# Kernel optimization log

Measured on AMD Instinct MI355X. Metric: run time of the kernel, lower is better.

Reference implementation:

```python
import jax, jax.numpy as jnp
import numpy as np

DIM = 512
HEADS = 8
HEAD_DIM = DIM // HEADS
SCALING = float(np.sqrt(HEAD_DIM))
B, S = 8, 2048


def setup_inputs() -> dict:
    key = jax.random.key(0)
    ks = jax.random.split(key, 6)
    x = jax.random.normal(ks[0], (B, S, DIM), dtype=jnp.float32)
    mask = jax.random.randint(ks[1], (B, S), 0, 2).astype(bool)
    mask = mask.at[:, 0].set(False)  # guarantee at least one unmasked key per row
    lim_qkv = 1.0 / np.sqrt(DIM)
    Wqkv = jax.random.uniform(ks[2], (3 * DIM, DIM), minval=-lim_qkv, maxval=lim_qkv, dtype=jnp.float32)
    bqkv = jax.random.uniform(ks[3], (3 * DIM,), minval=-lim_qkv, maxval=lim_qkv, dtype=jnp.float32)
    Wout = jax.random.uniform(ks[4], (DIM, DIM), minval=-lim_qkv, maxval=lim_qkv, dtype=jnp.float32)
    bout = jax.random.uniform(ks[5], (DIM,), minval=-lim_qkv, maxval=lim_qkv, dtype=jnp.float32)
    ln_g = jnp.ones((DIM,), dtype=jnp.float32)
    ln_b = jnp.zeros((DIM,), dtype=jnp.float32)
    return {"x": x, "mask": mask, "Wqkv": Wqkv, "bqkv": bqkv, "Wout": Wout, "bout": bout, "ln_g": ln_g, "ln_b": ln_b}


def reference(x, mask, Wqkv, bqkv, Wout, bout, ln_g, ln_b):
    b, s, _ = x.shape
    qkv = x @ Wqkv.T + bqkv                                   # [b, s, 3*dim]
    qkv = qkv.reshape(b, s, HEADS, HEAD_DIM, 3)               # torch reshape semantics (interleaved)
    q = qkv[..., 0]                                           # [b, s, h, d]
    k = qkv[..., 1]
    v = jax.nn.elu(qkv[..., 2])
    attn = jnp.einsum('bqhd,bkhd->bhqk', q, k) / SCALING      # [b, h, s, s]
    bias = jnp.where(mask[:, None, None, :], -jnp.inf, 0.0).astype(attn.dtype)
    attn = jax.nn.softmax(attn + bias, axis=-1)
    out = jnp.einsum('bhqk,bkhd->bqhd', attn, v).reshape(b, s, DIM)
    out = out @ Wout.T + bout
    mu = jnp.mean(out, axis=-1, keepdims=True)
    var = jnp.var(out, axis=-1, keepdims=True)
    out = (out - mu) / jnp.sqrt(var + 1e-5) * ln_g + ln_b
    return jax.nn.elu(out)
```

## Files before the change

kernel.cpp:

```cpp
#include <hip/hip_runtime.h>

#define DIM 512
#define HEADS 8
#define HD 64
#define NB 8
#define NS 2048
#define SCALE_INV 0.125f
#define NEG_BIG -1e30f
#define QSZ 8388608

typedef __attribute__((ext_vector_type(8))) short bf16x8;
typedef __attribute__((ext_vector_type(4))) float f32x4;

__device__ __forceinline__ float elu_f(float x) {
    return x > 0.0f ? x : (__expf(x) - 1.0f);
}
__device__ __forceinline__ short f2bf(float x) {
    union { float f; unsigned u; } v; v.f = x;
    unsigned r = v.u + 0x7FFFu + ((v.u >> 16) & 1u);
    return (short)(r >> 16);
}
__device__ __forceinline__ unsigned pack_bf_t(float a, float b) {
    union { float f; unsigned u; } va, vb; va.f = a; vb.f = b;
    return (va.u >> 16) | (vb.u & 0xFFFF0000u);
}

#define X4 2097152
#define W14 196608
#define W24 65536
__global__ __launch_bounds__(256) void prep(
    const float* __restrict__ x, const float* __restrict__ Wqkv,
    const float* __restrict__ bqkv, const float* __restrict__ Wout,
    short* __restrict__ xb, short* __restrict__ Wp,
    float* __restrict__ bp, short* __restrict__ Wob)
{
    int i = blockIdx.x * 256 + threadIdx.x;
    if (i < X4) {
        float4 v = *(const float4*)(x + (size_t)i * 4);
        ushort4 o; o.x = (unsigned short)f2bf(v.x); o.y = (unsigned short)f2bf(v.y);
        o.z = (unsigned short)f2bf(v.z); o.w = (unsigned short)f2bf(v.w);
        *(ushort4*)(xb + (size_t)i * 4) = o;
    } else if (i < X4 + W14) {
        int j = i - X4;
        int np = j >> 7, k = (j & 127) * 4;
        int w = np >> 9, h = (np >> 6) & 7, d = np & 63;
        int n = h * 192 + d * 3 + w;
        float4 v = *(const float4*)(Wqkv + (size_t)n * 512 + k);
        ushort4 o; o.x = (unsigned short)f2bf(v.x); o.y = (unsigned short)f2bf(v.y);
        o.z = (unsigned short)f2bf(v.z); o.w = (unsigned short)f2bf(v.w);
        *(ushort4*)(Wp + (size_t)np * 512 + k) = o;
    } else if (i < X4 + W14 + W24) {
        int j = i - X4 - W14;
        float4 v = *(const float4*)(Wout + (size_t)j * 4);
        ushort4 o; o.x = (unsigned short)f2bf(v.x); o.y = (unsigned short)f2bf(v.y);
        o.z = (unsigned short)f2bf(v.z); o.w = (unsigned short)f2bf(v.w);
        *(ushort4*)(Wob + (size_t)j * 4) = o;
    } else {
        int j = i - X4 - W14 - W24;
        int w = j >> 9, h = (j >> 6) & 7, d = j & 63;
        bp[j] = bqkv[h * 192 + d * 3 + w];
    }
}

__global__ __launch_bounds__(256) void qkv_mfma(
    const short* __restrict__ A, const short* __restrict__ Bw,
    const float* __restrict__ bp, short* __restrict__ QKV)
{
    __shared__ short smem[2 * 128 * 64];
    short* As = smem;
    short* Bs = smem + 128 * 64;
    const int t = threadIdx.x, lane = t & 63, wv = t >> 6;
    const int c = lane & 15, quad = lane >> 4;
    const int wr = wv >> 1, wc = wv & 1;
    const int m0 = blockIdx.x * 128, n0 = blockIdx.y * 128;
    f32x4 acc[4][4];
    #pragma unroll
    for (int mi = 0; mi < 4; ++mi)
        #pragma unroll
        for (int nj = 0; nj < 4; ++nj)
            #pragma unroll
            for (int i = 0; i < 4; ++i) acc[mi][nj][i] = 0.0f;

    for (int k0 = 0; k0 < 512; k0 += 64) {
        if (k0) __syncthreads();
        #pragma unroll
        for (int p = 0; p < 4; ++p) {
            int idx = p * 256 + t, r = idx >> 3, cb = idx & 7;
            *(uint4*)&As[r * 64 + ((cb ^ (r & 7)) * 8)] =
                *(const uint4*)(A + (size_t)(m0 + r) * 512 + k0 + cb * 8);
            *(uint4*)&Bs[r * 64 + ((cb ^ (r & 7)) * 8)] =
                *(const uint4*)(Bw + (size_t)(n0 + r) * 512 + k0 + cb * 8);
        }
        __syncthreads();
        bf16x8 af[4][2], bfr[4][2];
        #pragma unroll
        for (int mi = 0; mi < 4; ++mi) {
            int ar = wr * 64 + mi * 16 + c;
            af[mi][0] = *(const bf16x8*)&As[ar * 64 + ((quad       ^ (ar & 7)) * 8)];
            af[mi][1] = *(const bf16x8*)&As[ar * 64 + (((4 + quad) ^ (ar & 7)) * 8)];
        }
        #pragma unroll
        for (int nj = 0; nj < 4; ++nj) {
            int br = wc * 64 + nj * 16 + c;
            bfr[nj][0] = *(const bf16x8*)&Bs[br * 64 + ((quad       ^ (br & 7)) * 8)];
            bfr[nj][1] = *(const bf16x8*)&Bs[br * 64 + (((4 + quad) ^ (br & 7)) * 8)];
        }
        #pragma unroll
        for (int mi = 0; mi < 4; ++mi)
            #pragma unroll
            for (int nj = 0; nj < 4; ++nj) {
                acc[mi][nj] = __builtin_amdgcn_mfma_f32_16x16x32_bf16(af[mi][0], bfr[nj][0], acc[mi][nj], 0, 0, 0);
                acc[mi][nj] = __builtin_amdgcn_mfma_f32_16x16x32_bf16(af[mi][1], bfr[nj][1], acc[mi][nj], 0, 0, 0);
            }
    }

    const int w  = n0 >> 9;
    const int b  = m0 >> 11;
    const int hh = ((n0 + wc * 64) >> 6) & 7;
    float bv[4];
    #pragma unroll
    for (int nj = 0; nj < 4; ++nj) bv[nj] = bp[n0 + wc * 64 + nj * 16 + c];

    if (w < 2) {
        short* out = QKV + (size_t)w * QSZ + (size_t)(b * 8 + hh) * NS * 64;
        #pragma unroll
        for (int mi = 0; mi < 4; ++mi)
            #pragma unroll
            for (int i = 0; i < 4; ++i) {
                int s = (m0 & (NS - 1)) + wr * 64 + mi * 16 + quad * 4 + i;
                #pragma unroll
                for (int nj = 0; nj < 4; ++nj)
                    out[(size_t)s * 64 + nj * 16 + c] = f2bf(acc[mi][nj][i] + bv[nj]);
            }
    } else {
        __syncthreads();
        short* T = smem;
        #pragma unroll
        for (int mi = 0; mi < 4; ++mi)
            #pragma unroll
            for (int i = 0; i < 4; ++i) {
                int ml = wr * 64 + mi * 16 + quad * 4 + i;
                int mb = ml >> 3, mr = ml & 7;
                #pragma unroll
                for (int nj = 0; nj < 4; ++nj) {
                    int nl = wc * 64 + nj * 16 + c;
                    T[nl * 128 + ((mb ^ (nl & 15)) * 8) + mr] =
                        f2bf(elu_f(acc[mi][nj][i] + bv[nj]));
                }
            }
        __syncthreads();
        short* Vt = QKV + (size_t)2 * QSZ;
        #pragma unroll
        for (int p = 0; p < 8; ++p) {
            int idx = p * 256 + t, row = idx >> 4, ch = idx & 15;
            uint4 v = *(const uint4*)&T[row * 128 + ((ch ^ (row & 15)) * 8)];
            int d = row & 63;
            int h2 = ((n0 + row) >> 6) & 7;
            int sg = (m0 & (NS - 1)) + ch * 8;
            int kt = sg >> 6, ks = sg & 63;
            *(uint4*)(Vt + (((size_t)(b * 8 + h2) * 32 + kt) * 64 + d) * 64 + ks) = v;
        }
    }
}

__global__ __launch_bounds__(256, 4) void attn_mfma(
    const short* __restrict__ Qg, const short* __restrict__ Kg,
    const short* __restrict__ Vg, const int* __restrict__ mask,
    short* __restrict__ O)
{
    __shared__ short QP[64 * 64];
    __shared__ short Ks[64 * 64];
    __shared__ short Vs[64 * 64];
    __shared__ float msk[64];

    const int t = threadIdx.x;
    const int lane = t & 63;
    const int wv = t >> 6;
    const int c = lane & 15;
    const int quad = lane >> 4;
    const int bid = blockIdx.x;
    const int qt = bid & 31;
    const int h  = (bid >> 5) & 7;
    const int b  = bid >> 8;
    const int g  = b * 8 + h;
    const size_t base = (size_t)g * NS * HD;
    const int q0 = qt * 64;

    #pragma unroll
    for (int p = 0; p < 2; ++p) {
        int idx = p * 256 + t, r = idx >> 3, cb = idx & 7;
        *(uint4*)&QP[r * 64 + ((cb ^ (r & 7)) * 8)] =
            *(const uint4*)(Qg + base + (size_t)(q0 + r) * HD + cb * 8);
    }
    __syncthreads();

    const int mq = wv * 16 + c;
    const bf16x8 bq0 = *(const bf16x8*)&QP[mq * 64 + ((quad       ^ (mq & 7)) * 8)];
    const bf16x8 bq1 = *(const bf16x8*)&QP[mq * 64 + (((4 + quad) ^ (mq & 7)) * 8)];

    f32x4 o[4];
    #pragma unroll
    for (int dc = 0; dc < 4; ++dc)
        #pragma unroll
        for (int i = 0; i < 4; ++i) o[dc][i] = 0.0f;
    float lp = 0.0f;

    const int prow = wv * 16 + c;
    const int prot = 8 * (c & 7);

    for (int kt = 0; kt < 32; ++kt) {
        const int k0 = kt * 64;
        __syncthreads();
        #pragma unroll
        for (int p = 0; p < 2; ++p) {
            int idx = p * 256 + t, r = idx >> 3, cb = idx & 7;
            *(uint4*)&Ks[r * 64 + ((cb ^ (r & 7)) * 8)] =
                *(const uint4*)(Kg + base + (size_t)(k0 + r) * HD + cb * 8);
            *(uint4*)&Vs[r * 64 + (((cb * 8 + 8 * (r & 7)) & 63))] =
                *(const uint4*)(Vg + (((size_t)g * 32 + kt) * 64 + r) * 64 + cb * 8);
        }
        if (t < 64) msk[t] = mask[b * NS + k0 + t] ? NEG_BIG : 0.0f;
        __syncthreads();

        f32x4 st[4];
        #pragma unroll
        for (int ks = 0; ks < 4; ++ks) {
            int kr = ks * 16 + c;
            bf16x8 ak0 = *(const bf16x8*)&Ks[kr * 64 + ((quad       ^ (kr & 7)) * 8)];
            bf16x8 ak1 = *(const bf16x8*)&Ks[kr * 64 + (((4 + quad) ^ (kr & 7)) * 8)];
            f32x4 a = {0.0f, 0.0f, 0.0f, 0.0f};
            a = __builtin_amdgcn_mfma_f32_16x16x32_bf16(ak0, bq0, a, 0, 0, 0);
            a = __builtin_amdgcn_mfma_f32_16x16x32_bf16(ak1, bq1, a, 0, 0, 0);
            st[ks] = a;
        }

        #pragma unroll
        for (int ks = 0; ks < 4; ++ks) {
            float4 mb = *(const float4*)&msk[ks * 16 + quad * 4];
            float p0 = __expf(st[ks][0] * SCALE_INV + mb.x);
            float p1 = __expf(st[ks][1] * SCALE_INV + mb.y);
            float p2 = __expf(st[ks][2] * SCALE_INV + mb.z);
            float p3 = __expf(st[ks][3] * SCALE_INV + mb.w);
            lp += (p0 + p1) + (p2 + p3);
            uint2 pk;
            pk.x = pack_bf_t(p0, p1);
            pk.y = pack_bf_t(p2, p3);
            *(uint2*)&QP[prow * 64 + ((ks * 16 + quad * 4 + prot) & 63)] = pk;
        }

        bf16x8 bp0 = *(const bf16x8*)&QP[prow * 64 + ((quad * 8 + prot) & 63)];
        bf16x8 bp1 = *(const bf16x8*)&QP[prow * 64 + ((32 + quad * 8 + prot) & 63)];
        #pragma unroll
        for (int dc = 0; dc < 4; ++dc) {
            int d = dc * 16 + c;
            int vrot = 8 * (d & 7);
            bf16x8 av0 = *(const bf16x8*)&Vs[d * 64 + ((quad * 8 + vrot) & 63)];
            bf16x8 av1 = *(const bf16x8*)&Vs[d * 64 + ((32 + quad * 8 + vrot) & 63)];
            o[dc] = __builtin_amdgcn_mfma_f32_16x16x32_bf16(av0, bp0, o[dc], 0, 0, 0);
            o[dc] = __builtin_amdgcn_mfma_f32_16x16x32_bf16(av1, bp1, o[dc], 0, 0, 0);
        }
    }

    lp += __shfl_xor(lp, 16);
    lp += __shfl_xor(lp, 32);
    float inv = 1.0f / lp;

    int q = q0 + wv * 16 + c;
    short* orow = O + ((size_t)(b * NS + q)) * DIM + h * HD + quad * 4;
    #pragma unroll
    for (int dc = 0; dc < 4; ++dc) {
        uint2 pk;
        pk.x = (unsigned)(unsigned short)f2bf(o[dc][0] * inv)
             | ((unsigned)(unsigned short)f2bf(o[dc][1] * inv) << 16);
        pk.y = (unsigned)(unsigned short)f2bf(o[dc][2] * inv)
             | ((unsigned)(unsigned short)f2bf(o[dc][3] * inv) << 16);
        *(uint2*)(orow + dc * 16) = pk;
    }
}

__global__ __launch_bounds__(256) void out_mfma(
    const short* __restrict__ A, const short* __restrict__ Bw,
    const float* __restrict__ bias, float* __restrict__ Z)
{
    __shared__ short smem[2 * 128 * 64];
    short* As = smem;
    short* Bs = smem + 128 * 64;
    const int t = threadIdx.x, lane = t & 63, wv = t >> 6;
    const int c = lane & 15, quad = lane >> 4;
    const int wr = wv >> 1, wc = wv & 1;
    const int m0 = blockIdx.x * 128, n0 = blockIdx.y * 128;
    f32x4 acc[4][4];
    #pragma unroll
    for (int mi = 0; mi < 4; ++mi)
        #pragma unroll
        for (int nj = 0; nj < 4; ++nj)
            #pragma unroll
            for (int i = 0; i < 4; ++i) acc[mi][nj][i] = 0.0f;

    for (int k0 = 0; k0 < 512; k0 += 64) {
        if (k0) __syncthreads();
        #pragma unroll
        for (int p = 0; p < 4; ++p) {
            int idx = p * 256 + t, r = idx >> 3, cb = idx & 7;
            *(uint4*)&As[r * 64 + ((cb ^ (r & 7)) * 8)] =
                *(const uint4*)(A + (size_t)(m0 + r) * 512 + k0 + cb * 8);
            *(uint4*)&Bs[r * 64 + ((cb ^ (r & 7)) * 8)] =
                *(const uint4*)(Bw + (size_t)(n0 + r) * 512 + k0 + cb * 8);
        }
        __syncthreads();
        bf16x8 af[4][2], bfr[4][2];
        #pragma unroll
        for (int mi = 0; mi < 4; ++mi) {
            int ar = wr * 64 + mi * 16 + c;
            af[mi][0] = *(const bf16x8*)&As[ar * 64 + ((quad       ^ (ar & 7)) * 8)];
            af[mi][1] = *(const bf16x8*)&As[ar * 64 + (((4 + quad) ^ (ar & 7)) * 8)];
        }
        #pragma unroll
        for (int nj = 0; nj < 4; ++nj) {
            int br = wc * 64 + nj * 16 + c;
            bfr[nj][0] = *(const bf16x8*)&Bs[br * 64 + ((quad       ^ (br & 7)) * 8)];
            bfr[nj][1] = *(const bf16x8*)&Bs[br * 64 + (((4 + quad) ^ (br & 7)) * 8)];
        }
        #pragma unroll
        for (int mi = 0; mi < 4; ++mi)
            #pragma unroll
            for (int nj = 0; nj < 4; ++nj) {
                acc[mi][nj] = __builtin_amdgcn_mfma_f32_16x16x32_bf16(af[mi][0], bfr[nj][0], acc[mi][nj], 0, 0, 0);
                acc[mi][nj] = __builtin_amdgcn_mfma_f32_16x16x32_bf16(af[mi][1], bfr[nj][1], acc[mi][nj], 0, 0, 0);
            }
    }
    #pragma unroll
    for (int mi = 0; mi < 4; ++mi)
        #pragma unroll
        for (int i = 0; i < 4; ++i) {
            int mrow = m0 + wr * 64 + mi * 16 + quad * 4 + i;
            #pragma unroll
            for (int nj = 0; nj < 4; ++nj) {
                int n = n0 + wc * 64 + nj * 16 + c;
                Z[(size_t)mrow * 512 + n] = acc[mi][nj][i] + bias[n];
            }
        }
}

__global__ __launch_bounds__(256) void ln_elu(
    const float* __restrict__ Z, const float* __restrict__ g,
    const float* __restrict__ bt, float* __restrict__ out)
{
    const int row = blockIdx.x;
    const float* z = Z + (size_t)row * DIM;
    const int t = threadIdx.x;
    float v0 = z[t], v1 = z[t + 256];
    float s  = v0 + v1;
    float ss = v0 * v0 + v1 * v1;
    #pragma unroll
    for (int off = 32; off > 0; off >>= 1) {
        s  += __shfl_down(s, off);
        ss += __shfl_down(ss, off);
    }
    __shared__ float rs[4], rss[4];
    int wid = t >> 6, lane = t & 63;
    if (lane == 0) { rs[wid] = s; rss[wid] = ss; }
    __syncthreads();
    float S1 = rs[0] + rs[1] + rs[2] + rs[3];
    float S2 = rss[0] + rss[1] + rss[2] + rss[3];
    float mu  = S1 * (1.0f / DIM);
    float var = S2 * (1.0f / DIM) - mu * mu;
    float rstd = rsqrtf(var + 1e-5f);
    float y0 = (v0 - mu) * rstd * g[t]       + bt[t];
    float y1 = (v1 - mu) * rstd * g[t + 256] + bt[t + 256];
    out[(size_t)row * DIM + t]       = elu_f(y0);
    out[(size_t)row * DIM + t + 256] = elu_f(y1);
}

extern "C" void kernel_launch(void* const* d_in, const int* in_sizes, int n_in,
                              void* d_out, int out_size, void* d_ws, size_t ws_size,
                              hipStream_t stream)
{
    const float* x    = (const float*)d_in[0];
    const int*   mask = (const int*)d_in[1];
    const float* Wqkv = (const float*)d_in[2];
    const float* bqkv = (const float*)d_in[3];
    const float* Wout = (const float*)d_in[4];
    const float* bout = (const float*)d_in[5];
    const float* ln_g = (const float*)d_in[6];
    const float* ln_b = (const float*)d_in[7];
    float* out = (float*)d_out;

    short* xb   = (short*)d_ws;
    short* Wp   = xb + QSZ;
    short* Wob  = Wp + 786432;
    short* QKV  = Wob + 262144;
    short* ATTb = QKV + 3 * (size_t)QSZ;
    float* bp   = (float*)(ATTb + QSZ);
    float* Zb   = bp + 1536;

    prep<<<9222, 256, 0, stream>>>(x, Wqkv, bqkv, Wout, xb, Wp, bp, Wob);
    qkv_mfma<<<dim3(128, 12), 256, 0, stream>>>(xb, Wp, bp, QKV);
    attn_mfma<<<2048, 256, 0, stream>>>(QKV, QKV + QSZ, QKV + 2 * (size_t)QSZ, mask, ATTb);
    out_mfma<<<dim3(128, 4), 256, 0, stream>>>(ATTb, Wob, bout, Zb);
    ln_elu<<<NB * NS, 256, 0, stream>>>(Zb, ln_g, ln_b, out);
}
```

Before: 269.1 us.

## Give each attention wave two query sub-tiles to reuse K/V fragments

The attention block drops from 256 to 128 threads, and each wave now handles 32 query rows (two 16-row sub-tiles) instead of 16. The K and V LDS fragments are loaded once into registers and reused across both sub-tiles, which halves LDS reads per MFMA. It also swaps __expf for exp2f with a folded log2e*scale FMA and uses a larger masking constant. In exchange it raises register pressure, and with fewer waves per block there are fewer threads to cover latency and load tiles.

After: 361.3 us. +34.3%, slower.

```diff
diff --git a/kernel.cpp b/kernel.cpp
--- a/kernel.cpp
+++ b/kernel.cpp
@@ -6,6 +6,7 @@
 #define NB 8
 #define NS 2048
 #define SCALE_INV 0.125f
+#define LOG2E_SCALE 0.18033688011112042f
 #define NEG_BIG -1e30f
 #define QSZ 8388608
 
@@ -163,7 +164,7 @@
     }
 }
 
-__global__ __launch_bounds__(256, 4) void attn_mfma(
+__global__ __launch_bounds__(128, 3) void attn_mfma(
     const short* __restrict__ Qg, const short* __restrict__ Kg,
     const short* __restrict__ Vg, const int* __restrict__ mask,
     short* __restrict__ O)
@@ -187,94 +188,117 @@
     const int q0 = qt * 64;
 
     #pragma unroll
-    for (int p = 0; p < 2; ++p) {
-        int idx = p * 256 + t, r = idx >> 3, cb = idx & 7;
+    for (int p = 0; p < 4; ++p) {
+        int idx = p * 128 + t, r = idx >> 3, cb = idx & 7;
         *(uint4*)&QP[r * 64 + ((cb ^ (r & 7)) * 8)] =
             *(const uint4*)(Qg + base + (size_t)(q0 + r) * HD + cb * 8);
     }
     __syncthreads();
 
-    const int mq = wv * 16 + c;
-    const bf16x8 bq0 = *(const bf16x8*)&QP[mq * 64 + ((quad       ^ (mq & 7)) * 8)];
-    const bf16x8 bq1 = *(const bf16x8*)&QP[mq * 64 + (((4 + quad) ^ (mq & 7)) * 8)];
-
-    f32x4 o[4];
-    #pragma unroll
-    for (int dc = 0; dc < 4; ++dc)
-        #pragma unroll
-        for (int i = 0; i < 4; ++i) o[dc][i] = 0.0f;
-    float lp = 0.0f;
-
-    const int prow = wv * 16 + c;
+    bf16x8 bq[2][2];
+    #pragma unroll
+    for (int qs = 0; qs < 2; ++qs) {
+        int mq = wv * 32 + qs * 16 + c;
+        bq[qs][0] = *(const bf16x8*)&QP[mq * 64 + ((quad       ^ (mq & 7)) * 8)];
+        bq[qs][1] = *(const bf16x8*)&QP[mq * 64 + (((4 + quad) ^ (mq & 7)) * 8)];
+    }
+
+    f32x4 o[2][4];
+    #pragma unroll
+    for (int qs = 0; qs < 2; ++qs)
+        #pragma unroll
+        for (int dc = 0; dc < 4; ++dc)
+            #pragma unroll
+            for (int i = 0; i < 4; ++i) o[qs][dc][i] = 0.0f;
+    float lp[2] = {0.0f, 0.0f};
+
     const int prot = 8 * (c & 7);
 
     for (int kt = 0; kt < 32; ++kt) {
         const int k0 = kt * 64;
         __syncthreads();
         #pragma unroll
-        for (int p = 0; p < 2; ++p) {
-            int idx = p * 256 + t, r = idx >> 3, cb = idx & 7;
+        for (int p = 0; p < 4; ++p) {
+            int idx = p * 128 + t, r = idx >> 3, cb = idx & 7;
             *(uint4*)&Ks[r * 64 + ((cb ^ (r & 7)) * 8)] =
                 *(const uint4*)(Kg + base + (size_t)(k0 + r) * HD + cb * 8);
-            *(uint4*)&Vs[r * 64 + (((cb * 8 + 8 * (r & 7)) & 63))] =
+            *(uint4*)&Vs[r * 64 + ((cb * 8 + 8 * (r & 7)) & 63)] =
                 *(const uint4*)(Vg + (((size_t)g * 32 + kt) * 64 + r) * 64 + cb * 8);
         }
-        if (t < 64) msk[t] = mask[b * NS + k0 + t] ? NEG_BIG : 0.0f;
-        __syncthreads();
-
-        f32x4 st[4];
+        if (t < 64) msk[t] = mask[b * NS + k0 + t] ? -1e38f : 0.0f;
+        __syncthreads();
+
+        bf16x8 ak[4][2];
         #pragma unroll
         for (int ks = 0; ks < 4; ++ks) {
             int kr = ks * 16 + c;
-            bf16x8 ak0 = *(const bf16x8*)&Ks[kr * 64 + ((quad       ^ (kr & 7)) * 8)];
-            bf16x8 ak1 = *(const bf16x8*)&Ks[kr * 64 + (((4 + quad) ^ (kr & 7)) * 8)];
-            f32x4 a = {0.0f, 0.0f, 0.0f, 0.0f};
-            a = __builtin_amdgcn_mfma_f32_16x16x32_bf16(ak0, bq0, a, 0, 0, 0);
-            a = __builtin_amdgcn_mfma_f32_16x16x32_bf16(ak1, bq1, a, 0, 0, 0);
-            st[ks] = a;
-        }
-
-        #pragma unroll
-        for (int ks = 0; ks < 4; ++ks) {
-            float4 mb = *(const float4*)&msk[ks * 16 + quad * 4];
-            float p0 = __expf(st[ks][0] * SCALE_INV + mb.x);
-            float p1 = __expf(st[ks][1] * SCALE_INV + mb.y);
-            float p2 = __expf(st[ks][2] * SCALE_INV + mb.z);
-            float p3 = __expf(st[ks][3] * SCALE_INV + mb.w);
-            lp += (p0 + p1) + (p2 + p3);
-            uint2 pk;
-            pk.x = pack_bf_t(p0, p1);
-            pk.y = pack_bf_t(p2, p3);
-            *(uint2*)&QP[prow * 64 + ((ks * 16 + quad * 4 + prot) & 63)] = pk;
-        }
-
-        bf16x8 bp0 = *(const bf16x8*)&QP[prow * 64 + ((quad * 8 + prot) & 63)];
-        bf16x8 bp1 = *(const bf16x8*)&QP[prow * 64 + ((32 + quad * 8 + prot) & 63)];
+            ak[ks][0] = *(const bf16x8*)&Ks[kr * 64 + ((quad       ^ (kr & 7)) * 8)];
+            ak[ks][1] = *(const bf16x8*)&Ks[kr * 64 + (((4 + quad) ^ (kr & 7)) * 8)];
+        }
+
+        #pragma unroll
+        for (int qs = 0; qs < 2; ++qs) {
+            f32x4 st[4];
+            #pragma unroll
+            for (int ks = 0; ks < 4; ++ks) {
+                f32x4 a = {0.0f, 0.0f, 0.0f, 0.0f};
+                a = __builtin_amdgcn_mfma_f32_16x16x32_bf16(ak[ks][0], bq[qs][0], a, 0, 0, 0);
+                a = __builtin_amdgcn_mfma_f32_16x16x32_bf16(ak[ks][1], bq[qs][1], a, 0, 0, 0);
+                st[ks] = a;
+            }
+            const int prow = wv * 32 + qs * 16 + c;
+            #pragma unroll
+            for (int ks = 0; ks < 4; ++ks) {
+                float4 mb = *(const float4*)&msk[ks * 16 + quad * 4];
+                float p0 = exp2f(fmaf(st[ks][0], LOG2E_SCALE, mb.x));
+                float p1 = exp2f(fmaf(st[ks][1], LOG2E_SCALE, mb.y));
+                float p2 = exp2f(fmaf(st[ks][2], LOG2E_SCALE, mb.z));
+                float p3 = exp2f(fmaf(st[ks][3], LOG2E_SCALE, mb.w));
+                lp[qs] += (p0 + p1) + (p2 + p3);
+                uint2 pk;
+                pk.x = pack_bf_t(p0, p1);
+                pk.y = pack_bf_t(p2, p3);
+                *(uint2*)&QP[prow * 64 + ((ks * 16 + quad * 4 + prot) & 63)] = pk;
+            }
+        }
+
+        bf16x8 av[4][2];
         #pragma unroll
         for (int dc = 0; dc < 4; ++dc) {
             int d = dc * 16 + c;
-            int vrot = 8 * (d & 7);
-            bf16x8 av0 = *(const bf16x8*)&Vs[d * 64 + ((quad * 8 + vrot) & 63)];
-            bf16x8 av1 = *(const bf16x8*)&Vs[d * 64 + ((32 + quad * 8 + vrot) & 63)];
-            o[dc] = __builtin_amdgcn_mfma_f32_16x16x32_bf16(av0, bp0, o[dc], 0, 0, 0);
-            o[dc] = __builtin_amdgcn_mfma_f32_16x16x32_bf16(av1, bp1, o[dc], 0, 0, 0);
-        }
-    }
-
-    lp += __shfl_xor(lp, 16);
-    lp += __shfl_xor(lp, 32);
-    float inv = 1.0f / lp;
-
-    int q = q0 + wv * 16 + c;
-    short* orow = O + ((size_t)(b * NS + q)) * DIM + h * HD + quad * 4;
-    #pragma unroll
-    for (int dc = 0; dc < 4; ++dc) {
-        uint2 pk;
-        pk.x = (unsigned)(unsigned short)f2bf(o[dc][0] * inv)
-             | ((unsigned)(unsigned short)f2bf(o[dc][1] * inv) << 16);
-        pk.y = (unsigned)(unsigned short)f2bf(o[dc][2] * inv)
-             | ((unsigned)(unsigned short)f2bf(o[dc][3] * inv) << 16);
-        *(uint2*)(orow + dc * 16) = pk;
+            av[dc][0] = *(const bf16x8*)&Vs[d * 64 + ((quad * 8 + prot) & 63)];
+            av[dc][1] = *(const bf16x8*)&Vs[d * 64 + ((32 + quad * 8 + prot) & 63)];
+        }
+        #pragma unroll
+        for (int qs = 0; qs < 2; ++qs) {
+            const int prow = wv * 32 + qs * 16 + c;
+            bf16x8 bp0 = *(const bf16x8*)&QP[prow * 64 + ((quad * 8 + prot) & 63)];
+            bf16x8 bp1 = *(const bf16x8*)&QP[prow * 64 + ((32 + quad * 8 + prot) & 63)];
+            #pragma unroll
+            for (int dc = 0; dc < 4; ++dc) {
+                o[qs][dc] = __builtin_amdgcn_mfma_f32_16x16x32_bf16(av[dc][0], bp0, o[qs][dc], 0, 0, 0);
+                o[qs][dc] = __builtin_amdgcn_mfma_f32_16x16x32_bf16(av[dc][1], bp1, o[qs][dc], 0, 0, 0);
+            }
+        }
+    }
+
+    #pragma unroll
+    for (int qs = 0; qs < 2; ++qs) {
+        float ls = lp[qs];
+        ls += __shfl_xor(ls, 16);
+        ls += __shfl_xor(ls, 32);
+        float inv = 1.0f / ls;
+        int q = q0 + wv * 32 + qs * 16 + c;
+        short* orow = O + ((size_t)(b * NS + q)) * DIM + h * HD + quad * 4;
+        #pragma unroll
+        for (int dc = 0; dc < 4; ++dc) {
+            uint2 pk;
+            pk.x = (unsigned)(unsigned short)f2bf(o[qs][dc][0] * inv)
+                 | ((unsigned)(unsigned short)f2bf(o[qs][dc][1] * inv) << 16);
+            pk.y = (unsigned)(unsigned short)f2bf(o[qs][dc][2] * inv)
+                 | ((unsigned)(unsigned short)f2bf(o[qs][dc][3] * inv) << 16);
+            *(uint2*)(orow + dc * 16) = pk;
+        }
     }
 }
 
@@ -396,7 +420,7 @@
 
     prep<<<9222, 256, 0, stream>>>(x, Wqkv, bqkv, Wout, xb, Wp, bp, Wob);
     qkv_mfma<<<dim3(128, 12), 256, 0, stream>>>(xb, Wp, bp, QKV);
-    attn_mfma<<<2048, 256, 0, stream>>>(QKV, QKV + QSZ, QKV + 2 * (size_t)QSZ, mask, ATTb);
+    attn_mfma<<<2048, 128, 0, stream>>>(QKV, QKV + QSZ, QKV + 2 * (size_t)QSZ, mask, ATTb);
     out_mfma<<<dim3(128, 4), 256, 0, stream>>>(ATTb, Wob, bout, Zb);
     ln_elu<<<NB * NS, 256, 0, stream>>>(Zb, ln_g, ln_b, out);
 }
```

## Fuse output projection with LayerNorm and ELU in one kernel

Applied to the files above, without the earlier changes.

Replaces the separate output GEMM and LayerNorm+ELU kernels with one kernel where each block computes full 512-wide rows for 32 tokens, reduces mean and variance in registers and shared memory, and writes the final output directly. This removes the fp32 intermediate Z round trip through global memory and one kernel launch. In exchange, B fragments are loaded straight from global memory without LDS staging, and the grid shrinks to 512 blocks with 32-row tiles, which lowers reuse of the A and B tiles.

Result: slower. 277.1 us (+3.0%).

```diff
diff --git a/kernel.cpp b/kernel.cpp
--- a/kernel.cpp
+++ b/kernel.cpp
@@ -278,98 +278,110 @@
     }
 }
 
-__global__ __launch_bounds__(256) void out_mfma(
+__global__ __launch_bounds__(256) void out_ln(
     const short* __restrict__ A, const short* __restrict__ Bw,
-    const float* __restrict__ bias, float* __restrict__ Z)
+    const float* __restrict__ bias, const float* __restrict__ lg,
+    const float* __restrict__ lb, float* __restrict__ out)
 {
-    __shared__ short smem[2 * 128 * 64];
-    short* As = smem;
-    short* Bs = smem + 128 * 64;
+    __shared__ short As[32 * 64];
+    __shared__ float rs[4][32], rss[4][32];
     const int t = threadIdx.x, lane = t & 63, wv = t >> 6;
     const int c = lane & 15, quad = lane >> 4;
-    const int wr = wv >> 1, wc = wv & 1;
-    const int m0 = blockIdx.x * 128, n0 = blockIdx.y * 128;
-    f32x4 acc[4][4];
-    #pragma unroll
-    for (int mi = 0; mi < 4; ++mi)
-        #pragma unroll
-        for (int nj = 0; nj < 4; ++nj)
+    const int m0 = blockIdx.x * 32;
+    f32x4 acc[2][8];
+    #pragma unroll
+    for (int mi = 0; mi < 2; ++mi)
+        #pragma unroll
+        for (int nj = 0; nj < 8; ++nj)
             #pragma unroll
             for (int i = 0; i < 4; ++i) acc[mi][nj][i] = 0.0f;
 
     for (int k0 = 0; k0 < 512; k0 += 64) {
         if (k0) __syncthreads();
-        #pragma unroll
-        for (int p = 0; p < 4; ++p) {
-            int idx = p * 256 + t, r = idx >> 3, cb = idx & 7;
+        {
+            int r = t >> 3, cb = t & 7;
             *(uint4*)&As[r * 64 + ((cb ^ (r & 7)) * 8)] =
                 *(const uint4*)(A + (size_t)(m0 + r) * 512 + k0 + cb * 8);
-            *(uint4*)&Bs[r * 64 + ((cb ^ (r & 7)) * 8)] =
-                *(const uint4*)(Bw + (size_t)(n0 + r) * 512 + k0 + cb * 8);
-        }
-        __syncthreads();
-        bf16x8 af[4][2], bfr[4][2];
-        #pragma unroll
-        for (int mi = 0; mi < 4; ++mi) {
-            int ar = wr * 64 + mi * 16 + c;
+        }
+        __syncthreads();
+        bf16x8 af[2][2];
+        #pragma unroll
+        for (int mi = 0; mi < 2; ++mi) {
+            int ar = mi * 16 + c;
             af[mi][0] = *(const bf16x8*)&As[ar * 64 + ((quad       ^ (ar & 7)) * 8)];
             af[mi][1] = *(const bf16x8*)&As[ar * 64 + (((4 + quad) ^ (ar & 7)) * 8)];
         }
         #pragma unroll
-        for (int nj = 0; nj < 4; ++nj) {
-            int br = wc * 64 + nj * 16 + c;
-            bfr[nj][0] = *(const bf16x8*)&Bs[br * 64 + ((quad       ^ (br & 7)) * 8)];
-            bfr[nj][1] = *(const bf16x8*)&Bs[br * 64 + (((4 + quad) ^ (br & 7)) * 8)];
-        }
-        #pragma unroll
-        for (int mi = 0; mi < 4; ++mi)
-            #pragma unroll
-            for (int nj = 0; nj < 4; ++nj) {
-                acc[mi][nj] = __builtin_amdgcn_mfma_f32_16x16x32_bf16(af[mi][0], bfr[nj][0], acc[mi][nj], 0, 0, 0);
-                acc[mi][nj] = __builtin_amdgcn_mfma_f32_16x16x32_bf16(af[mi][1], bfr[nj][1], acc[mi][nj], 0, 0, 0);
-            }
-    }
-    #pragma unroll
-    for (int mi = 0; mi < 4; ++mi)
+        for (int nj = 0; nj < 8; ++nj) {
+            int n = wv * 128 + nj * 16 + c;
+            bf16x8 b0 = *(const bf16x8*)(Bw + (size_t)n * 512 + k0 + quad * 8);
+            bf16x8 b1 = *(const bf16x8*)(Bw + (size_t)n * 512 + k0 + 32 + quad * 8);
+            #pragma unroll
+            for (int mi = 0; mi < 2; ++mi) {
+                acc[mi][nj] = __builtin_amdgcn_mfma_f32_16x16x32_bf16(af[mi][0], b0, acc[mi][nj], 0, 0, 0);
+                acc[mi][nj] = __builtin_amdgcn_mfma_f32_16x16x32_bf16(af[mi][1], b1, acc[mi][nj], 0, 0, 0);
+            }
+        }
+    }
+
+    float bv[8];
+    #pragma unroll
+    for (int nj = 0; nj < 8; ++nj) bv[nj] = bias[wv * 128 + nj * 16 + c];
+    float s_[2][4], ss_[2][4];
+    #pragma unroll
+    for (int mi = 0; mi < 2; ++mi)
         #pragma unroll
         for (int i = 0; i < 4; ++i) {
-            int mrow = m0 + wr * 64 + mi * 16 + quad * 4 + i;
-            #pragma unroll
-            for (int nj = 0; nj < 4; ++nj) {
-                int n = n0 + wc * 64 + nj * 16 + c;
-                Z[(size_t)mrow * 512 + n] = acc[mi][nj][i] + bias[n];
-            }
-        }
-}
-
-__global__ __launch_bounds__(256) void ln_elu(
-    const float* __restrict__ Z, const float* __restrict__ g,
-    const float* __restrict__ bt, float* __restrict__ out)
-{
-    const int row = blockIdx.x;
-    const float* z = Z + (size_t)row * DIM;
-    const int t = threadIdx.x;
-    float v0 = z[t], v1 = z[t + 256];
-    float s  = v0 + v1;
-    float ss = v0 * v0 + v1 * v1;
-    #pragma unroll
-    for (int off = 32; off > 0; off >>= 1) {
-        s  += __shfl_down(s, off);
-        ss += __shfl_down(ss, off);
-    }
-    __shared__ float rs[4], rss[4];
-    int wid = t >> 6, lane = t & 63;
-    if (lane == 0) { rs[wid] = s; rss[wid] = ss; }
+            float s = 0.0f, ss = 0.0f;
+            #pragma unroll
+            for (int nj = 0; nj < 8; ++nj) {
+                float z = acc[mi][nj][i] + bv[nj];
+                acc[mi][nj][i] = z;
+                s += z; ss += z * z;
+            }
+            #pragma unroll
+            for (int off = 1; off < 16; off <<= 1) {
+                s  += __shfl_xor(s, off);
+                ss += __shfl_xor(ss, off);
+            }
+            s_[mi][i] = s; ss_[mi][i] = ss;
+        }
+    if (c == 0) {
+        #pragma unroll
+        for (int mi = 0; mi < 2; ++mi)
+            #pragma unroll
+            for (int i = 0; i < 4; ++i) {
+                int row = mi * 16 + quad * 4 + i;
+                rs[wv][row] = s_[mi][i];
+                rss[wv][row] = ss_[mi][i];
+            }
+    }
     __syncthreads();
-    float S1 = rs[0] + rs[1] + rs[2] + rs[3];
-    float S2 = rss[0] + rss[1] + rss[2] + rss[3];
-    float mu  = S1 * (1.0f / DIM);
-    float var = S2 * (1.0f / DIM) - mu * mu;
-    float rstd = rsqrtf(var + 1e-5f);
-    float y0 = (v0 - mu) * rstd * g[t]       + bt[t];
-    float y1 = (v1 - mu) * rstd * g[t + 256] + bt[t + 256];
-    out[(size_t)row * DIM + t]       = elu_f(y0);
-    out[(size_t)row * DIM + t + 256] = elu_f(y1);
+
+    float gv[8], bbv[8];
+    #pragma unroll
+    for (int nj = 0; nj < 8; ++nj) {
+        int n = wv * 128 + nj * 16 + c;
+        gv[nj] = lg[n]; bbv[nj] = lb[n];
+    }
+    #pragma unroll
+    for (int mi = 0; mi < 2; ++mi)
+        #pragma unroll
+        for (int i = 0; i < 4; ++i) {
+            int row = mi * 16 + quad * 4 + i;
+            float S1 = rs[0][row] + rs[1][row] + rs[2][row] + rs[3][row];
+            float S2 = rss[0][row] + rss[1][row] + rss[2][row] + rss[3][row];
+            float mu = S1 * (1.0f / DIM);
+            float var = S2 * (1.0f / DIM) - mu * mu;
+            float rstd = rsqrtf(var + 1e-5f);
+            float* orow = out + (size_t)(m0 + row) * DIM;
+            #pragma unroll
+            for (int nj = 0; nj < 8; ++nj) {
+                int n = wv * 128 + nj * 16 + c;
+                float y = (acc[mi][nj][i] - mu) * rstd * gv[nj] + bbv[nj];
+                orow[n] = elu_f(y);
+            }
+        }
 }
 
 extern "C" void kernel_launch(void* const* d_in, const int* in_sizes, int n_in,
@@ -392,11 +404,9 @@
     short* QKV  = Wob + 262144;
     short* ATTb = QKV + 3 * (size_t)QSZ;
     float* bp   = (float*)(ATTb + QSZ);
-    float* Zb   = bp + 1536;
 
     prep<<<9222, 256, 0, stream>>>(x, Wqkv, bqkv, Wout, xb, Wp, bp, Wob);
     qkv_mfma<<<dim3(128, 12), 256, 0, stream>>>(xb, Wp, bp, QKV);
     attn_mfma<<<2048, 256, 0, stream>>>(QKV, QKV + QSZ, QKV + 2 * (size_t)QSZ, mask, ATTb);
-    out_mfma<<<dim3(128, 4), 256, 0, stream>>>(ATTb, Wob, bout, Zb);
-    ln_elu<<<NB * NS, 256, 0, stream>>>(Zb, ln_g, ln_b, out);
-}
+    out_ln<<<512, 256, 0, stream>>>(ATTb, Wob, bout, ln_g, ln_b, out);
+}
```
